# Optimization experiments

Measured on AMD Instinct MI355X. Metric: run time of the kernel, lower is better.

## Reference

```python
import jax, jax.numpy as jnp
import numpy as np


def setup_inputs() -> dict:
    key = jax.random.key(0)
    x = jax.random.normal(key, (4, 4, 32, 256, 256), dtype=jnp.float32)
    return {"x": x}


def reference(x):
    # NonMaximaSuppression3d with kernel_size=(3,3,3) fast path:
    # a voxel survives iff it is strictly greater than all 26 neighbors;
    # border voxels (no full neighborhood) are always suppressed.
    B, CH, D, H, W = x.shape
    ct = x[..., 1:-1, 1:-1, 1:-1]  # interior centers [B,CH,D-2,H-2,W-2]
    mask_inner = jnp.ones(ct.shape, dtype=bool)
    for dz in range(3):
        for dy in range(3):
            for dx in range(3):
                if (dz, dy, dx) == (1, 1, 1):
                    continue
                neigh = x[..., dz:D - 2 + dz, dy:H - 2 + dy, dx:W - 2 + dx]
                mask_inner = mask_inner & (ct > neigh)
    mask = jnp.zeros(x.shape, dtype=bool).at[..., 1:-1, 1:-1, 1:-1].set(mask_inner)
    return x * mask.astype(x.dtype)
```

## Files before the change

kernel.cpp:

```cpp
#include <hip/hip_runtime.h>


typedef float v4f __attribute__((ext_vector_type(4)));

constexpr int W  = 256;
constexpr int H  = 256;
constexpr int D  = 32;
constexpr int SH = W;
constexpr int SD = W * H;
constexpr int HC = 8;
constexpr int NR = HC + 2;
constexpr int NSLOT = 4;
constexpr int BC = 16;
constexpr int HG = H / HC;
constexpr int SPLIT = 2;
constexpr int DR = D / SPLIT;
constexpr int PLW = NR * W;

__device__ __forceinline__ v4f vmax4(v4f a, v4f b) {
    return (v4f){fmaxf(a.x, b.x), fmaxf(a.y, b.y), fmaxf(a.z, b.z), fmaxf(a.w, b.w)};
}

__device__ __forceinline__ void stage_plane(const float* __restrict__ vol,
                                            float* lds, int p, int h0,
                                            int wv, int lane) {
    const int pc = p < 0 ? 0 : (p > D - 1 ? D - 1 : p);
    float* dst = lds + (p & 3) * PLW;
    const float* src = vol + pc * SD + (lane << 2);
    {
        int hh = h0 - 1 + wv; hh = hh < 0 ? 0 : hh;
        __builtin_amdgcn_global_load_lds(
            (const __attribute__((address_space(1))) unsigned int*)(src + hh * SH),
            (__attribute__((address_space(3))) unsigned int*)(dst + wv * W), 16, 0, 0);
    }
    {
        const int hh = h0 - 1 + wv + 4;
        __builtin_amdgcn_global_load_lds(
            (const __attribute__((address_space(1))) unsigned int*)(src + hh * SH),
            (__attribute__((address_space(3))) unsigned int*)(dst + (wv + 4) * W), 16, 0, 0);
    }
    if (wv < 2) {
        int hh = h0 - 1 + wv + 8; hh = hh > H - 1 ? H - 1 : hh;
        __builtin_amdgcn_global_load_lds(
            (const __attribute__((address_space(1))) unsigned int*)(src + hh * SH),
            (__attribute__((address_space(3))) unsigned int*)(dst + (wv + 8) * W), 16, 0, 0);
    }
}

__device__ __forceinline__ v4f nms_row(v4f m0, v4f m1, v4f m2,
                                       v4f c0, v4f c1, v4f c2,
                                       v4f p0, v4f p1, v4f p2,
                                       bool valid, int lane) {
    const v4f a3m = vmax4(vmax4(m0, m1), m2);
    const v4f a3p = vmax4(vmax4(p0, p1), p2);
    const v4f a20 = vmax4(c0, c2);
    const v4f v8  = vmax4(vmax4(a3m, a3p), a20);
    const v4f c   = c1;

    const float l8 = __shfl_up(v8.w, 1);
    const float r8 = __shfl_down(v8.x, 1);
    const float lc = __shfl_up(c.w, 1);
    const float rc = __shfl_down(c.x, 1);

    float n0 = fmaxf(fmaxf(l8,   v8.x), v8.y);
    float n1 = fmaxf(fmaxf(v8.x, v8.y), v8.z);
    float n2 = fmaxf(fmaxf(v8.y, v8.z), v8.w);
    float n3 = fmaxf(fmaxf(v8.z, v8.w), r8);
    n0 = fmaxf(n0, fmaxf(lc,  c.y));
    n1 = fmaxf(n1, fmaxf(c.x, c.z));
    n2 = fmaxf(n2, fmaxf(c.y, c.w));
    n3 = fmaxf(n3, fmaxf(c.z, rc));

    v4f o;
    o.x = (valid && lane > 0  && c.x > n0) ? c.x : 0.f;
    o.y = (valid && c.y > n1) ? c.y : 0.f;
    o.z = (valid && c.z > n2) ? c.z : 0.f;
    o.w = (valid && lane < 63 && c.w > n3) ? c.w : 0.f;
    return o;
}

__global__ __launch_bounds__(256, 4) void nms3d_kernel(const float* __restrict__ x,
                                                       float* __restrict__ out) {
    __shared__ float lds[NSLOT * PLW];

    const int blk  = blockIdx.x;
    const int wv   = threadIdx.x >> 6;
    const int lane = threadIdx.x & 63;
    const int hc   = blk & (HG - 1);
    const int half = (blk >> 5) & (SPLIT - 1);
    const int bc   = blk >> 6;
    const int d0   = half * DR;
    const int h0   = hc * HC;

    const float* vol  = x   + bc * (D * SD);
    float*       ovol = out + bc * (D * SD);

    stage_plane(vol, lds, d0 - 1, h0, wv, lane);
    stage_plane(vol, lds, d0,     h0, wv, lane);
    stage_plane(vol, lds, d0 + 1, h0, wv, lane);
    __syncthreads();

    const int i0 = wv * 2;
    const int h  = h0 + i0;
    const bool hv0 = (h > 0) && (h < H - 1);
    const bool hv1 = (h + 1 < H - 1);

    #pragma unroll 1
    for (int d = d0; d < d0 + DR; ++d) {
        stage_plane(vol, lds, d + 2, h0, wv, lane);

        const bool dv = (d > 0) && (d < D - 1);
        const float* Lm = lds + ((d - 1) & 3) * PLW + i0 * W + (lane << 2);
        const float* L0 = lds + ( d      & 3) * PLW + i0 * W + (lane << 2);
        const float* Lp = lds + ((d + 1) & 3) * PLW + i0 * W + (lane << 2);

        const v4f m0 = *(const v4f*)(Lm + 0 * W), m1 = *(const v4f*)(Lm + 1 * W);
        const v4f m2 = *(const v4f*)(Lm + 2 * W), m3 = *(const v4f*)(Lm + 3 * W);
        const v4f c0 = *(const v4f*)(L0 + 0 * W), c1 = *(const v4f*)(L0 + 1 * W);
        const v4f c2 = *(const v4f*)(L0 + 2 * W), c3 = *(const v4f*)(L0 + 3 * W);
        const v4f p0 = *(const v4f*)(Lp + 0 * W), p1 = *(const v4f*)(Lp + 1 * W);
        const v4f p2 = *(const v4f*)(Lp + 2 * W), p3 = *(const v4f*)(Lp + 3 * W);

        float* orow = ovol + d * SD + h * SH + (lane << 2);
        const v4f o0 = nms_row(m0, m1, m2, c0, c1, c2, p0, p1, p2, hv0 && dv, lane);
        __builtin_nontemporal_store(o0, (v4f*)orow);
        const v4f o1 = nms_row(m1, m2, m3, c1, c2, c3, p1, p2, p3, hv1 && dv, lane);
        __builtin_nontemporal_store(o1, (v4f*)(orow + SH));

        __syncthreads();
    }
}

extern "C" void kernel_launch(void* const* d_in, const int* in_sizes, int n_in,
                              void* d_out, int out_size, void* d_ws, size_t ws_size,
                              hipStream_t stream) {
    const float* x = (const float*)d_in[0];
    float* out = (float*)d_out;
    const int grid = BC * HG * SPLIT;
    nms3d_kernel<<<grid, 256, 0, stream>>>(x, out);
}
```

Measured before the change: 241.6 us.

## Replace depth-streaming LDS ring with one-shot small 3D tiles per block

Each block now loads a 4-plane by 6-row halo tile into LDS in a single pass and computes 2 depth planes by 4 rows, instead of streaming 16 planes through a rotating 4-slot buffer. The grid grows from 1024 to 16384 blocks and the occupancy hint rises, removing the per-plane barrier loop and exposing more memory-level parallelism. The trade-off is a higher halo re-read ratio (24 rows loaded for 8 output rows), which relies on L2 to absorb the redundant global traffic.

```diff
diff --git a/kernel.cpp b/kernel.cpp
--- a/kernel.cpp
+++ b/kernel.cpp
@@ -8,43 +8,17 @@
 constexpr int D  = 32;
 constexpr int SH = W;
 constexpr int SD = W * H;
-constexpr int HC = 8;
-constexpr int NR = HC + 2;
-constexpr int NSLOT = 4;
+constexpr int KD = 2;
+constexpr int HC = 4;
 constexpr int BC = 16;
+constexpr int DG = D / KD;
 constexpr int HG = H / HC;
-constexpr int SPLIT = 2;
-constexpr int DR = D / SPLIT;
-constexpr int PLW = NR * W;
+constexpr int NPL = KD + 2;
+constexpr int NR  = HC + 2;
+constexpr int TROWS = NPL * NR;
 
 __device__ __forceinline__ v4f vmax4(v4f a, v4f b) {
     return (v4f){fmaxf(a.x, b.x), fmaxf(a.y, b.y), fmaxf(a.z, b.z), fmaxf(a.w, b.w)};
-}
-
-__device__ __forceinline__ void stage_plane(const float* __restrict__ vol,
-                                            float* lds, int p, int h0,
-                                            int wv, int lane) {
-    const int pc = p < 0 ? 0 : (p > D - 1 ? D - 1 : p);
-    float* dst = lds + (p & 3) * PLW;
-    const float* src = vol + pc * SD + (lane << 2);
-    {
-        int hh = h0 - 1 + wv; hh = hh < 0 ? 0 : hh;
-        __builtin_amdgcn_global_load_lds(
-            (const __attribute__((address_space(1))) unsigned int*)(src + hh * SH),
-            (__attribute__((address_space(3))) unsigned int*)(dst + wv * W), 16, 0, 0);
-    }
-    {
-        const int hh = h0 - 1 + wv + 4;
-        __builtin_amdgcn_global_load_lds(
-            (const __attribute__((address_space(1))) unsigned int*)(src + hh * SH),
-            (__attribute__((address_space(3))) unsigned int*)(dst + (wv + 4) * W), 16, 0, 0);
-    }
-    if (wv < 2) {
-        int hh = h0 - 1 + wv + 8; hh = hh > H - 1 ? H - 1 : hh;
-        __builtin_amdgcn_global_load_lds(
-            (const __attribute__((address_space(1))) unsigned int*)(src + hh * SH),
-            (__attribute__((address_space(3))) unsigned int*)(dst + (wv + 8) * W), 16, 0, 0);
-    }
 }
 
 __device__ __forceinline__ v4f nms_row(v4f m0, v4f m1, v4f m2,
@@ -79,56 +53,60 @@
     return o;
 }
 
-__global__ __launch_bounds__(256, 4) void nms3d_kernel(const float* __restrict__ x,
+__global__ __launch_bounds__(256, 6) void nms3d_kernel(const float* __restrict__ x,
                                                        float* __restrict__ out) {
-    __shared__ float lds[NSLOT * PLW];
+    __shared__ float lds[TROWS * W];
 
     const int blk  = blockIdx.x;
     const int wv   = threadIdx.x >> 6;
     const int lane = threadIdx.x & 63;
     const int hc   = blk & (HG - 1);
-    const int half = (blk >> 5) & (SPLIT - 1);
-    const int bc   = blk >> 6;
-    const int d0   = half * DR;
+    const int dg   = (blk >> 6) & (DG - 1);
+    const int bc   = blk >> 10;
+    const int d0   = dg * KD;
     const int h0   = hc * HC;
 
-    const float* vol  = x   + bc * (D * SD);
-    float*       ovol = out + bc * (D * SD);
+    const float* vol = x + bc * (D * SD);
 
-    stage_plane(vol, lds, d0 - 1, h0, wv, lane);
-    stage_plane(vol, lds, d0,     h0, wv, lane);
-    stage_plane(vol, lds, d0 + 1, h0, wv, lane);
+    {
+        int p = d0 - 1 + wv;  p = p < 0 ? 0 : (p > D - 1 ? D - 1 : p);
+        const float* src = vol + p * SD + (lane << 2);
+        float* dst = &lds[(wv * NR) * W];
+        #pragma unroll
+        for (int r = 0; r < NR; ++r) {
+            int hh = h0 - 1 + r; hh = hh < 0 ? 0 : (hh > H - 1 ? H - 1 : hh);
+            __builtin_amdgcn_global_load_lds(
+                (const __attribute__((address_space(1))) unsigned int*)(src + hh * SH),
+                (__attribute__((address_space(3))) unsigned int*)(dst + r * W),
+                16, 0, 0);
+        }
+    }
     __syncthreads();
 
-    const int i0 = wv * 2;
-    const int h  = h0 + i0;
+    const int pi = wv >> 1;
+    const int r0 = (wv & 1) * 2;
+    const int d  = d0 + pi;
+    const bool dv = (d > 0) && (d < D - 1);
+    const int h  = h0 + r0;
     const bool hv0 = (h > 0) && (h < H - 1);
     const bool hv1 = (h + 1 < H - 1);
 
-    #pragma unroll 1
-    for (int d = d0; d < d0 + DR; ++d) {
-        stage_plane(vol, lds, d + 2, h0, wv, lane);
+    const float* Lm = lds + (pi * NR + r0) * W + (lane << 2);
+    const float* L0 = Lm + NR * W;
+    const float* Lp = L0 + NR * W;
 
-        const bool dv = (d > 0) && (d < D - 1);
-        const float* Lm = lds + ((d - 1) & 3) * PLW + i0 * W + (lane << 2);
-        const float* L0 = lds + ( d      & 3) * PLW + i0 * W + (lane << 2);
-        const float* Lp = lds + ((d + 1) & 3) * PLW + i0 * W + (lane << 2);
+    const v4f m0 = *(const v4f*)(Lm + 0 * W), m1 = *(const v4f*)(Lm + 1 * W);
+    const v4f m2 = *(const v4f*)(Lm + 2 * W), m3 = *(const v4f*)(Lm + 3 * W);
+    const v4f c0 = *(const v4f*)(L0 + 0 * W), c1 = *(const v4f*)(L0 + 1 * W);
+    const v4f c2 = *(const v4f*)(L0 + 2 * W), c3 = *(const v4f*)(L0 + 3 * W);
+    const v4f p0 = *(const v4f*)(Lp + 0 * W), p1 = *(const v4f*)(Lp + 1 * W);
+    const v4f p2 = *(const v4f*)(Lp + 2 * W), p3 = *(const v4f*)(Lp + 3 * W);
 
-        const v4f m0 = *(const v4f*)(Lm + 0 * W), m1 = *(const v4f*)(Lm + 1 * W);
-        const v4f m2 = *(const v4f*)(Lm + 2 * W), m3 = *(const v4f*)(Lm + 3 * W);
-        const v4f c0 = *(const v4f*)(L0 + 0 * W), c1 = *(const v4f*)(L0 + 1 * W);
-        const v4f c2 = *(const v4f*)(L0 + 2 * W), c3 = *(const v4f*)(L0 + 3 * W);
-        const v4f p0 = *(const v4f*)(Lp + 0 * W), p1 = *(const v4f*)(Lp + 1 * W);
-        const v4f p2 = *(const v4f*)(Lp + 2 * W), p3 = *(const v4f*)(Lp + 3 * W);
-
-        float* orow = ovol + d * SD + h * SH + (lane << 2);
-        const v4f o0 = nms_row(m0, m1, m2, c0, c1, c2, p0, p1, p2, hv0 && dv, lane);
-        __builtin_nontemporal_store(o0, (v4f*)orow);
-        const v4f o1 = nms_row(m1, m2, m3, c1, c2, c3, p1, p2, p3, hv1 && dv, lane);
-        __builtin_nontemporal_store(o1, (v4f*)(orow + SH));
-
-        __syncthreads();
-    }
+    float* orow = out + bc * (D * SD) + d * SD + h * SH + (lane << 2);
+    const v4f o0 = nms_row(m0, m1, m2, c0, c1, c2, p0, p1, p2, hv0 && dv, lane);
+    __builtin_nontemporal_store(o0, (v4f*)orow);
+    const v4f o1 = nms_row(m1, m2, m3, c1, c2, c3, p1, p2, p3, hv1 && dv, lane);
+    __builtin_nontemporal_store(o1, (v4f*)(orow + SH));
 }
 
 extern "C" void kernel_launch(void* const* d_in, const int* in_sizes, int n_in,
@@ -136,6 +114,6 @@
                               hipStream_t stream) {
     const float* x = (const float*)d_in[0];
     float* out = (float*)d_out;
-    const int grid = BC * HG * SPLIT;
+    const int grid = BC * DG * HG;
     nms3d_kernel<<<grid, 256, 0, stream>>>(x, out);
 }
```

After: 223.8 us. 1.08x faster.
